# Kernel optimization log

Measured on AMD Instinct MI355X. Metric: run time of the kernel, lower is better.

The kernel has to match this reference:

```python
import jax, jax.numpy as jnp
import numpy as np

EPS = 1e-7
K_CURV = 1.0                       # init_curvature buffer
HOPFIELD_DIM = 128
BETA = 1.0 / HOPFIELD_DIM ** 0.5   # default beta = 1/sqrt(hopfield_dim)


def _to_tangent0(x):
    # prepend zero time coordinate, clip max norm to 3.5
    zeros = jnp.zeros(x.shape[:-1] + (1,), dtype=x.dtype)
    x = jnp.concatenate([zeros, x], axis=-1)
    n = jnp.linalg.norm(x, axis=-1, keepdims=True)
    factor = jnp.minimum(3.5 / (n + EPS), 1.0)
    return x * factor


def _linner(u, v):
    # Minkowski (Lorentz) inner product: -u0*v0 + sum_i ui*vi
    return -u[..., 0] * v[..., 0] + jnp.sum(u[..., 1:] * v[..., 1:], axis=-1)


def _expmap0(u, k):
    # exp map at hyperboloid origin; u has zero time component
    sk = jnp.sqrt(k)
    xs = u[..., 1:]
    n = jnp.maximum(jnp.linalg.norm(xs, axis=-1, keepdims=True), EPS)
    t = n / sk
    return jnp.concatenate([sk * jnp.cosh(t), sk * jnp.sinh(t) * xs / n], axis=-1)


def _logmap(x, y, k):
    # log map of y in tangent space at x
    xy = _linner(x, y)[..., None]
    dist = jnp.sqrt(k) * jnp.arccosh(jnp.maximum(-xy / k, 1.0 + EPS))
    nomin = y + (xy / k) * x
    denom = jnp.sqrt(jnp.maximum(_linner(nomin, nomin)[..., None], EPS))
    return dist * nomin / denom


def _expmap(x, u, k):
    # exp map of tangent vector u at base point x
    sk = jnp.sqrt(k)
    un = jnp.sqrt(jnp.maximum(_linner(u, u)[..., None], EPS))
    t = un / sk
    return jnp.cosh(t) * x + sk * jnp.sinh(t) * u / un


def _logmap0(x, k):
    # log map at origin; time component of the result is zero
    sk = jnp.sqrt(k)
    xs = x[..., 1:]
    n = jnp.maximum(jnp.linalg.norm(xs, axis=-1, keepdims=True), EPS)
    dist = sk * jnp.arccosh(jnp.maximum(x[..., :1] / sk, 1.0 + EPS))
    return jnp.concatenate([jnp.zeros_like(x[..., :1]), dist * xs / n], axis=-1)


def setup_inputs() -> dict:
    key = jax.random.key(0)
    k1, k2, k3, k4, k5 = jax.random.split(key, 5)
    N, M, D_MEM, D_H, D_OUT = 1024, 2048, 512, 128, 128
    return {
        "queries": jax.random.normal(k1, (N, D_H), dtype=jnp.float32),
        "keys": jax.random.normal(k2, (M, D_MEM), dtype=jnp.float32),
        "values": jax.random.normal(k3, (M, D_MEM), dtype=jnp.float32),
        "W_K": jax.random.normal(k4, (D_MEM, D_H), dtype=jnp.float32) * 0.05,
        "W_V": jax.random.normal(k5, (D_H, D_OUT), dtype=jnp.float32) * 0.05,
    }


def reference(queries, keys, values, W_K, W_V):
    k = K_CURV
    Q = _expmap0(_to_tangent0(queries), k)              # [N, D+1]
    K = _expmap0(_to_tangent0(keys @ W_K), k)           # [M, D+1]
    V = _expmap0(_to_tangent0((values @ W_K) @ W_V), k) # [M, D+1]
    sim = _linner(Q[:, None, :], K[None, :, :])         # [N, M]
    alpha = jax.nn.softmax(-BETA * sim, axis=-1)        # [N, M]
    log_values = _logmap(Q[:, None, :], V[None, :, :], k)  # [N, M, D+1]
    tangent_mean = jnp.sum(alpha[..., None] * log_values, axis=1)  # [N, D+1]
    z = _expmap(Q, tangent_mean, k)
    return _logmap0(z, k)[..., 1:]                      # [N, D]
```

## Files before the change

### kernel.cpp

```cpp
#include <hip/hip_runtime.h>
#include <math.h>

#define EPSF 1e-7f
#define BETA_F 0.08838834764831845f

typedef __attribute__((ext_vector_type(8))) short bf8_t;
typedef __attribute__((ext_vector_type(4))) float f32x4;

#define WS_QT    0
#define WS_LQ    1024
#define WS_KT    2048
#define WS_VTM   4096
#define WS_LV    6144
#define WS_QS    8192
#define WS_QHI   139264
#define WS_QLO   204800
#define WS_KHI   270336
#define WS_KLO   401408
#define WS_VHI   532480
#define WS_VLO   663552
#define WS_VTHI  794624
#define WS_VTLO  925696
#define WS_WKT0  1056768
#define WS_WKT1  1089536
#define WS_WKT2  1122304
#define WS_WVT0  1155072
#define WS_WVT1  1163264
#define WS_WVT2  1171456
#define WS_PART  1179648

__device__ __forceinline__ float wave_sum(float v) {
#pragma unroll
  for (int off = 32; off > 0; off >>= 1) v += __shfl_xor(v, off);
  return v;
}
__device__ __forceinline__ unsigned short f2bf(float x) {
  unsigned int u = __float_as_uint(x);
  u += 0x7FFFu + ((u >> 16) & 1u);
  return (unsigned short)(u >> 16);
}
__device__ __forceinline__ float bf2f(unsigned short h) {
  return __uint_as_float(((unsigned int)h) << 16);
}
__device__ __forceinline__ void split3(float x, unsigned short& s0, unsigned short& s1,
                                       unsigned short& s2) {
  s0 = f2bf(x);
  float r1 = x - bf2f(s0);
  s1 = f2bf(r1);
  s2 = f2bf(r1 - bf2f(s1));
}
__device__ __forceinline__ bf8_t ld8(const unsigned short* p) {
  return __builtin_bit_cast(bf8_t, *(const uint4*)p);
}
__device__ __forceinline__ f32x4 mfma16(bf8_t a, bf8_t b, f32x4 c) {
  return __builtin_amdgcn_mfma_f32_16x16x32_bf16(a, b, c, 0, 0, 0);
}

__global__ void prep_q(const float* __restrict__ queries, float* __restrict__ Qs,
                       float* __restrict__ qt, float* __restrict__ lqv,
                       unsigned int* __restrict__ Qhi, unsigned int* __restrict__ Qlo) {
  int i = blockIdx.x;
  int lane = threadIdx.x;
  float2 r = ((const float2*)(queries + (size_t)i * 128))[lane];
  float s2 = wave_sum(r.x * r.x + r.y * r.y);
  float n = sqrtf(s2);
  float f = fminf(3.5f / (n + EPSF), 1.0f);
  float t = fmaxf(n * f, EPSF);
  float coef = sinhf(t) / t * f;
  float ch = coshf(t);
  float x0 = coef * r.x, x1 = coef * r.y;
  ((float2*)(Qs + (size_t)i * 128))[lane] = make_float2(x0, x1);
  unsigned short h0 = f2bf(x0), h1 = f2bf(x1);
  Qhi[i * 64 + lane] = (unsigned)h0 | ((unsigned)h1 << 16);
  unsigned short g0 = f2bf(x0 - bf2f(h0)), g1 = f2bf(x1 - bf2f(h1));
  Qlo[i * 64 + lane] = (unsigned)g0 | ((unsigned)g1 << 16);
  if (lane == 0) {
    qt[i] = ch;
    lqv[i] = coef * coef * s2 - ch * ch;
  }
}

__global__ void convert_w(const float* __restrict__ WK, const float* __restrict__ WV,
                          unsigned short* __restrict__ WKT0, unsigned short* __restrict__ WKT1,
                          unsigned short* __restrict__ WKT2,
                          unsigned short* __restrict__ WVT0, unsigned short* __restrict__ WVT1,
                          unsigned short* __restrict__ WVT2) {
  int t = blockIdx.x * 256 + threadIdx.x;
  if (t < 65536) {
    int n = t >> 9, k = t & 511;
    unsigned short a, b, c;
    split3(WK[k * 128 + n], a, b, c);
    WKT0[t] = a; WKT1[t] = b; WKT2[t] = c;
  } else {
    int t2 = t - 65536;
    int n = t2 >> 7, k = t2 & 127;
    unsigned short a, b, c;
    split3(WV[k * 128 + n], a, b, c);
    WVT0[t2] = a; WVT1[t2] = b; WVT2[t2] = c;
  }
}

__launch_bounds__(512)
__global__ void prep_kv(const float* __restrict__ keys, const float* __restrict__ values,
                        const unsigned short* __restrict__ WKT0,
                        const unsigned short* __restrict__ WKT1,
                        const unsigned short* __restrict__ WKT2,
                        const unsigned short* __restrict__ WVT0,
                        const unsigned short* __restrict__ WVT1,
                        const unsigned short* __restrict__ WVT2,
                        unsigned short* __restrict__ Khi, unsigned short* __restrict__ Klo,
                        float* __restrict__ kt,
                        unsigned short* __restrict__ Vhi, unsigned short* __restrict__ Vlo,
                        unsigned short* __restrict__ VThi, unsigned short* __restrict__ VTlo,
                        float* __restrict__ vt, float* __restrict__ lv) {
  int tid = threadIdx.x, wv = tid >> 6, lane = tid & 63;
  int l15 = lane & 15, lh = lane >> 4;
  int b = blockIdx.x;
  bool isK = b < 128;
  int r0 = (b & 127) * 16;
  const float* src = isK ? keys : values;

  __shared__ __align__(16) float ldsD[16][132];
  __shared__ __align__(16) unsigned short v1p[3][16][128];
  __shared__ __align__(16) float ldsD2[16][132];
  __shared__ __align__(16) float ldsT[128][17];

  f32x4 acc = f32x4{0, 0, 0, 0};
  const float* arow = src + (size_t)(r0 + l15) * 512 + lh * 8;
#pragma unroll 2
  for (int ks = 0; ks < 16; ++ks) {
    float4 a0 = *(const float4*)(arow + ks * 32);
    float4 a1 = *(const float4*)(arow + ks * 32 + 4);
    float av[8] = {a0.x, a0.y, a0.z, a0.w, a1.x, a1.y, a1.z, a1.w};
    bf8_t aa0, aa1, aa2;
#pragma unroll
    for (int i = 0; i < 8; ++i) {
      unsigned short p0, p1, p2;
      split3(av[i], p0, p1, p2);
      aa0[i] = (short)p0; aa1[i] = (short)p1; aa2[i] = (short)p2;
    }
    size_t boff = (size_t)(wv * 16 + l15) * 512 + ks * 32 + lh * 8;
    bf8_t b0 = ld8(WKT0 + boff);
    bf8_t b1 = ld8(WKT1 + boff);
    bf8_t b2 = ld8(WKT2 + boff);
    acc = mfma16(aa0, b0, acc);
    acc = mfma16(aa0, b1, acc);
    acc = mfma16(aa1, b0, acc);
    acc = mfma16(aa0, b2, acc);
    acc = mfma16(aa1, b1, acc);
    acc = mfma16(aa2, b0, acc);
  }
#pragma unroll
  for (int r = 0; r < 4; ++r) ldsD[lh * 4 + r][wv * 16 + l15] = acc[r];
  __syncthreads();

  if (isK) {
    if (tid < 256) {
      int row = tid >> 4, l = tid & 15;
      float a[8];
#pragma unroll
      for (int n = 0; n < 8; ++n) a[n] = ldsD[row][n * 16 + l];
      float s2 = 0.f;
#pragma unroll
      for (int n = 0; n < 8; ++n) s2 += a[n] * a[n];
#pragma unroll
      for (int off = 1; off < 16; off <<= 1) s2 += __shfl_xor(s2, off);
      float nn = sqrtf(s2);
      float f = fminf(3.5f / (nn + EPSF), 1.0f);
      float t = fmaxf(nn * f, EPSF);
      float coef = sinhf(t) / t * f;
      if (l == 0) kt[r0 + row] = coshf(t);
#pragma unroll
      for (int n = 0; n < 8; ++n) {
        float sv = coef * a[n];
        unsigned short h = f2bf(sv);
        Khi[(size_t)(r0 + row) * 128 + n * 16 + l] = h;
        Klo[(size_t)(r0 + row) * 128 + n * 16 + l] = f2bf(sv - bf2f(h));
      }
    }
    return;
  }

  if (tid < 256) {
    int row = tid >> 4, l = tid & 15;
#pragma unroll
    for (int n = 0; n < 8; ++n) {
      unsigned short p0, p1, p2;
      split3(ldsD[row][n * 16 + l], p0, p1, p2);
      v1p[0][row][n * 16 + l] = p0;
      v1p[1][row][n * 16 + l] = p1;
      v1p[2][row][n * 16 + l] = p2;
    }
  }
  __syncthreads();

  f32x4 a2 = f32x4{0, 0, 0, 0};
#pragma unroll
  for (int ks = 0; ks < 4; ++ks) {
    bf8_t x0 = ld8(&v1p[0][l15][ks * 32 + lh * 8]);
    bf8_t x1 = ld8(&v1p[1][l15][ks * 32 + lh * 8]);
    bf8_t x2 = ld8(&v1p[2][l15][ks * 32 + lh * 8]);
    size_t boff = (size_t)(wv * 16 + l15) * 128 + ks * 32 + lh * 8;
    bf8_t b0 = ld8(WVT0 + boff);
    bf8_t b1 = ld8(WVT1 + boff);
    bf8_t b2 = ld8(WVT2 + boff);
    a2 = mfma16(x0, b0, a2);
    a2 = mfma16(x0, b1, a2);
    a2 = mfma16(x1, b0, a2);
    a2 = mfma16(x0, b2, a2);
    a2 = mfma16(x1, b1, a2);
    a2 = mfma16(x2, b0, a2);
  }
#pragma unroll
  for (int r = 0; r < 4; ++r) ldsD2[lh * 4 + r][wv * 16 + l15] = a2[r];
  __syncthreads();

  if (tid < 256) {
    int row = tid >> 4, l = tid & 15;
    float a[8];
#pragma unroll
    for (int n = 0; n < 8; ++n) a[n] = ldsD2[row][n * 16 + l];
    float s2 = 0.f;
#pragma unroll
    for (int n = 0; n < 8; ++n) s2 += a[n] * a[n];
#pragma unroll
    for (int off = 1; off < 16; off <<= 1) s2 += __shfl_xor(s2, off);
    float nn = sqrtf(s2);
    float f = fminf(3.5f / (nn + EPSF), 1.0f);
    float t = fmaxf(nn * f, EPSF);
    float coef = sinhf(t) / t * f;
    float ch = coshf(t);
    if (l == 0) {
      vt[r0 + row] = ch;
      lv[r0 + row] = coef * coef * s2 - ch * ch;
    }
#pragma unroll
    for (int n = 0; n < 8; ++n) {
      float sv = coef * a[n];
      unsigned short h = f2bf(sv);
      Vhi[(size_t)(r0 + row) * 128 + n * 16 + l] = h;
      Vlo[(size_t)(r0 + row) * 128 + n * 16 + l] = f2bf(sv - bf2f(h));
      ldsT[n * 16 + l][row] = sv;
    }
  }
  __syncthreads();

  if (tid < 128) {
    int d = tid;
    unsigned int wh[8], wl[8];
#pragma unroll
    for (int i = 0; i < 8; ++i) {
      float s0 = ldsT[d][2 * i], s1 = ldsT[d][2 * i + 1];
      unsigned short h0 = f2bf(s0), h1 = f2bf(s1);
      unsigned short g0 = f2bf(s0 - bf2f(h0)), g1 = f2bf(s1 - bf2f(h1));
      wh[i] = (unsigned)h0 | ((unsigned)h1 << 16);
      wl[i] = (unsigned)g0 | ((unsigned)g1 << 16);
    }
    size_t o = (size_t)d * 2048 + r0;
    *(uint4*)(VThi + o) = make_uint4(wh[0], wh[1], wh[2], wh[3]);
    *(uint4*)(VThi + o + 8) = make_uint4(wh[4], wh[5], wh[6], wh[7]);
    *(uint4*)(VTlo + o) = make_uint4(wl[0], wl[1], wl[2], wl[3]);
    *(uint4*)(VTlo + o + 8) = make_uint4(wl[4], wl[5], wl[6], wl[7]);
  }
}

__launch_bounds__(256, 2)
__global__ void attn_mfma(const unsigned short* __restrict__ Qhi, const unsigned short* __restrict__ Qlo,
                          const unsigned short* __restrict__ Khi, const unsigned short* __restrict__ Klo,
                          const unsigned short* __restrict__ Vhi, const unsigned short* __restrict__ Vlo,
                          const unsigned short* __restrict__ VThi, const unsigned short* __restrict__ VTlo,
                          const float* __restrict__ qt, const float* __restrict__ lqv,
                          const float* __restrict__ kt, const float* __restrict__ vt,
                          const float* __restrict__ lv, float* __restrict__ part) {
  int tid = threadIdx.x, wv = tid >> 6, lane = tid & 63;
  int l15 = lane & 15, lh = lane >> 4;
  int qg = blockIdx.x >> 3, sp = blockIdx.x & 7;
  int q0 = qg * 16;
  int j0 = sp * 256 + wv * 64;

  __shared__ __align__(16) unsigned short ghA[4][1024];
  __shared__ __align__(16) unsigned short glA[4][1024];
  __shared__ __align__(16) float mergeO[4][16][132];
  __shared__ float mergeS[4][3][16];

  bf8_t qfh[4], qfl[4];
  {
    const unsigned short* qp = Qhi + (size_t)(q0 + l15) * 128 + lh * 8;
    const unsigned short* ql = Qlo + (size_t)(q0 + l15) * 128 + lh * 8;
#pragma unroll
    for (int ks = 0; ks < 4; ++ks) { qfh[ks] = ld8(qp + ks * 32); qfl[ks] = ld8(ql + ks * 32); }
  }
  float qtr[4], lq2[4];
#pragma unroll
  for (int r = 0; r < 4; ++r) {
    int q = q0 + lh * 4 + r;
    qtr[r] = qt[q];
    lq2[r] = 2.0f + lqv[q];
  }
  float ktj[4], vtj[4], lvj[4];
#pragma unroll
  for (int n = 0; n < 4; ++n) {
    int j = j0 + n * 16 + l15;
    ktj[n] = kt[j]; vtj[n] = vt[j]; lvj[n] = lv[j];
  }

  auto loadT = [&](bf8_t* st, int nn) {
    size_t jrow = (size_t)(j0 + nn * 16 + l15) * 128 + lh * 8;
#pragma unroll
    for (int ks = 0; ks < 4; ++ks) {
      st[ks * 4 + 0] = ld8(Khi + jrow + ks * 32);
      st[ks * 4 + 1] = ld8(Klo + jrow + ks * 32);
      st[ks * 4 + 2] = ld8(Vhi + jrow + ks * 32);
      st[ks * 4 + 3] = ld8(Vlo + jrow + ks * 32);
    }
  };
  auto mfmaT = [&](const bf8_t* st, f32x4& s, f32x4& c) {
#pragma unroll
    for (int ks = 0; ks < 4; ++ks) {
      s = mfma16(qfh[ks], st[ks * 4 + 0], s);
      s = mfma16(qfh[ks], st[ks * 4 + 1], s);
      s = mfma16(qfl[ks], st[ks * 4 + 0], s);
      c = mfma16(qfh[ks], st[ks * 4 + 2], c);
      c = mfma16(qfh[ks], st[ks * 4 + 3], c);
      c = mfma16(qfl[ks], st[ks * 4 + 2], c);
    }
  };
  f32x4 sf[4], cf[4];
#pragma unroll
  for (int n = 0; n < 4; ++n) { sf[n] = f32x4{0, 0, 0, 0}; cf[n] = f32x4{0, 0, 0, 0}; }
  bf8_t stA[16], stB[16];
  loadT(stA, 0);
  loadT(stB, 1);
  mfmaT(stA, sf[0], cf[0]);
  loadT(stA, 2);
  mfmaT(stB, sf[1], cf[1]);
  loadT(stB, 3);
  mfmaT(stA, sf[2], cf[2]);
  mfmaT(stB, sf[3], cf[3]);

  bf8_t vA[16], vB[16];
  auto loadV = [&](bf8_t* st, int jk) {
#pragma unroll
    for (int dn = 0; dn < 8; ++dn) {
      size_t vrow = (size_t)(dn * 16 + l15) * 2048 + j0 + jk * 32 + lh * 8;
      st[dn * 2 + 0] = ld8(VThi + vrow);
      st[dn * 2 + 1] = ld8(VTlo + vrow);
    }
  };
  loadV(vA, 0);

  float lsum[4] = {0, 0, 0, 0}, tcs[4] = {0, 0, 0, 0}, tts[4] = {0, 0, 0, 0};
#pragma unroll
  for (int n = 0; n < 4; ++n) {
#pragma unroll
    for (int r = 0; r < 4; ++r) {
      float sim = sf[n][r] - qtr[r] * ktj[n];
      float c = cf[n][r] - qtr[r] * vtj[n];
      float e = expf(-BETA_F * sim);
      float z = fmaxf(-c, 1.0f + EPSF);
      float dist = acoshf(z);
      float den2 = fmaxf(lvj[n] + lq2[r] * c * c, EPSF);
      float g = e * dist * rsqrtf(den2);
      lsum[r] += e;
      tcs[r] += g * c;
      tts[r] += g * vtj[n];
      unsigned short gh = f2bf(g);
      unsigned short gl = f2bf(g - bf2f(gh));
      int q_ = lh * 4 + r;
      int idx = (q_ * 64 + n * 16 + l15) ^ ((q_ & 7) << 3);
      ghA[wv][idx] = gh;
      glA[wv][idx] = gl;
    }
  }
  loadV(vB, 1);
  asm volatile("s_waitcnt lgkmcnt(0)" ::: "memory");
  __builtin_amdgcn_sched_barrier(0);

  f32x4 accO[8];
#pragma unroll
  for (int dn = 0; dn < 8; ++dn) accO[dn] = f32x4{0, 0, 0, 0};
  {
    int base0 = (l15 * 64 + 0 * 32 + lh * 8) ^ ((l15 & 7) << 3);
    bf8_t ah = ld8(&ghA[wv][base0]);
    bf8_t al = ld8(&glA[wv][base0]);
#pragma unroll
    for (int dn = 0; dn < 8; ++dn) {
      accO[dn] = mfma16(ah, vA[dn * 2 + 0], accO[dn]);
      accO[dn] = mfma16(ah, vA[dn * 2 + 1], accO[dn]);
      accO[dn] = mfma16(al, vA[dn * 2 + 0], accO[dn]);
    }
  }
  {
    int base1 = (l15 * 64 + 1 * 32 + lh * 8) ^ ((l15 & 7) << 3);
    bf8_t ah = ld8(&ghA[wv][base1]);
    bf8_t al = ld8(&glA[wv][base1]);
#pragma unroll
    for (int dn = 0; dn < 8; ++dn) {
      accO[dn] = mfma16(ah, vB[dn * 2 + 0], accO[dn]);
      accO[dn] = mfma16(ah, vB[dn * 2 + 1], accO[dn]);
      accO[dn] = mfma16(al, vB[dn * 2 + 0], accO[dn]);
    }
  }

#pragma unroll
  for (int r = 0; r < 4; ++r) {
#pragma unroll
    for (int off = 1; off < 16; off <<= 1) {
      lsum[r] += __shfl_xor(lsum[r], off);
      tcs[r] += __shfl_xor(tcs[r], off);
      tts[r] += __shfl_xor(tts[r], off);
    }
  }

#pragma unroll
  for (int r = 0; r < 4; ++r) {
    int q_ = lh * 4 + r;
#pragma unroll
    for (int dn = 0; dn < 8; ++dn) mergeO[wv][q_][dn * 16 + l15] = accO[dn][r];
    if (l15 == 0) {
      mergeS[wv][0][q_] = lsum[r];
      mergeS[wv][1][q_] = tcs[r];
      mergeS[wv][2][q_] = tts[r];
    }
  }
  __syncthreads();

#pragma unroll
  for (int e = 0; e < 2; ++e) {
    int t = tid + e * 256;
    int q_ = t >> 5, d0 = (t & 31) * 4;
    float4 s = make_float4(0.f, 0.f, 0.f, 0.f);
#pragma unroll
    for (int w = 0; w < 4; ++w) {
      float4 v = *(const float4*)&mergeO[w][q_][d0];
      s.x += v.x; s.y += v.y; s.z += v.z; s.w += v.w;
    }
    float* P = part + ((size_t)(q0 + q_) * 8 + sp) * 132;
    *(float4*)(P + d0) = s;
  }
  if (tid < 16) {
    int q_ = tid;
    float a = 0, b = 0, cc2 = 0;
#pragma unroll
    for (int w = 0; w < 4; ++w) {
      a += mergeS[w][0][q_];
      b += mergeS[w][1][q_];
      cc2 += mergeS[w][2][q_];
    }
    float* P = part + ((size_t)(q0 + q_) * 8 + sp) * 132;
    P[128] = a; P[129] = b; P[130] = cc2;
  }
}

__global__ void merge_fin(const float* __restrict__ part, const float* __restrict__ Qs,
                          const float* __restrict__ qt, float* __restrict__ out) {
  int qi = blockIdx.x;
  int lane = threadIdx.x;
  const float* P = part + (size_t)qi * 8 * 132;
  float ox = 0, oy = 0, l = 0, tc = 0, tt = 0;
#pragma unroll
  for (int s = 0; s < 8; ++s) {
    const float* p = P + s * 132;
    float2 o2 = *(const float2*)(p + 2 * lane);
    ox += o2.x; oy += o2.y;
    l += p[128]; tc += p[129]; tt += p[130];
  }
  float2 q2 = ((const float2*)(Qs + (size_t)qi * 128))[lane];
  float qtv = qt[qi];
  float invl = 1.0f / l;
  float Tmx = (ox + tc * q2.x) * invl;
  float Tmy = (oy + tc * q2.y) * invl;
  float Tmt = (tt + tc * qtv) * invl;
  float sp2 = wave_sum(Tmx * Tmx + Tmy * Tmy);
  float LT = sp2 - Tmt * Tmt;
  float un = sqrtf(fmaxf(LT, EPSF));
  float ch = coshf(un);
  float shv = sinhf(un) / un;
  float zx = ch * q2.x + shv * Tmx;
  float zy = ch * q2.y + shv * Tmy;
  float zt = ch * qtv + shv * Tmt;
  float zn2 = wave_sum(zx * zx + zy * zy);
  float nz = fmaxf(sqrtf(zn2), EPSF);
  float dist = acoshf(fmaxf(zt, 1.0f + EPSF));
  float sc = dist / nz;
  ((float2*)(out + (size_t)qi * 128))[lane] = make_float2(sc * zx, sc * zy);
}

extern "C" void kernel_launch(void* const* d_in, const int* in_sizes, int n_in,
                              void* d_out, int out_size, void* d_ws, size_t ws_size,
                              hipStream_t stream) {
  const float* queries = (const float*)d_in[0];
  const float* keys = (const float*)d_in[1];
  const float* values = (const float*)d_in[2];
  const float* WK = (const float*)d_in[3];
  const float* WV = (const float*)d_in[4];
  float* ws = (float*)d_ws;

  float* qt_ = ws + WS_QT;
  float* lq_ = ws + WS_LQ;
  float* kt_ = ws + WS_KT;
  float* vt_ = ws + WS_VTM;
  float* lv_ = ws + WS_LV;
  float* Qs = ws + WS_QS;
  unsigned short* Qhi = (unsigned short*)(ws + WS_QHI);
  unsigned short* Qlo = (unsigned short*)(ws + WS_QLO);
  unsigned short* Khi = (unsigned short*)(ws + WS_KHI);
  unsigned short* Klo = (unsigned short*)(ws + WS_KLO);
  unsigned short* Vhi = (unsigned short*)(ws + WS_VHI);
  unsigned short* Vlo = (unsigned short*)(ws + WS_VLO);
  unsigned short* VThi = (unsigned short*)(ws + WS_VTHI);
  unsigned short* VTlo = (unsigned short*)(ws + WS_VTLO);
  unsigned short* WKT0 = (unsigned short*)(ws + WS_WKT0);
  unsigned short* WKT1 = (unsigned short*)(ws + WS_WKT1);
  unsigned short* WKT2 = (unsigned short*)(ws + WS_WKT2);
  unsigned short* WVT0 = (unsigned short*)(ws + WS_WVT0);
  unsigned short* WVT1 = (unsigned short*)(ws + WS_WVT1);
  unsigned short* WVT2 = (unsigned short*)(ws + WS_WVT2);
  float* part = ws + WS_PART;
  float* out = (float*)d_out;

  prep_q<<<1024, 64, 0, stream>>>(queries, Qs, qt_, lq_, (unsigned int*)Qhi, (unsigned int*)Qlo);
  convert_w<<<320, 256, 0, stream>>>(WK, WV, WKT0, WKT1, WKT2, WVT0, WVT1, WVT2);
  prep_kv<<<256, 512, 0, stream>>>(keys, values, WKT0, WKT1, WKT2, WVT0, WVT1, WVT2,
                                   Khi, Klo, kt_, Vhi, Vlo, VThi, VTlo, vt_, lv_);
  attn_mfma<<<512, 256, 0, stream>>>(Qhi, Qlo, Khi, Klo, Vhi, Vlo, VThi, VTlo,
                                     qt_, lq_, kt_, vt_, lv_, part);
  merge_fin<<<1024, 64, 0, stream>>>(part, Qs, qt_, out);
}
```

Before: 70.49 us.

## Halve prep_kv rows per block, tile weight transpose through LDS, prefetch A loads

Result: slower. 88.72 us (+25.9%).

```diff
diff --git a/kernel.cpp b/kernel.cpp
--- a/kernel.cpp
+++ b/kernel.cpp
@@ -85,18 +85,43 @@
                           unsigned short* __restrict__ WKT2,
                           unsigned short* __restrict__ WVT0, unsigned short* __restrict__ WVT1,
                           unsigned short* __restrict__ WVT2) {
-  int t = blockIdx.x * 256 + threadIdx.x;
-  if (t < 65536) {
-    int n = t >> 9, k = t & 511;
-    unsigned short a, b, c;
-    split3(WK[k * 128 + n], a, b, c);
-    WKT0[t] = a; WKT1[t] = b; WKT2[t] = c;
+  __shared__ float tile[64][65];
+  int b = blockIdx.x, tid = threadIdx.x;
+  if (b < 16) {
+    int kt = b >> 1, nt = b & 1;
+    int c0 = tid & 63, r0 = tid >> 6;
+#pragma unroll
+    for (int i = 0; i < 16; ++i) {
+      int kr = r0 + i * 4;
+      tile[kr][c0] = WK[(size_t)(kt * 64 + kr) * 128 + nt * 64 + c0];
+    }
+    __syncthreads();
+#pragma unroll
+    for (int i = 0; i < 16; ++i) {
+      int nr = r0 + i * 4;
+      unsigned short a, bb, c;
+      split3(tile[c0][nr], a, bb, c);
+      size_t o = (size_t)(nt * 64 + nr) * 512 + kt * 64 + c0;
+      WKT0[o] = a; WKT1[o] = bb; WKT2[o] = c;
+    }
   } else {
-    int t2 = t - 65536;
-    int n = t2 >> 7, k = t2 & 127;
-    unsigned short a, b, c;
-    split3(WV[k * 128 + n], a, b, c);
-    WVT0[t2] = a; WVT1[t2] = b; WVT2[t2] = c;
+    int b2 = b - 16;
+    int kt = b2 >> 1, nt = b2 & 1;
+    int c0 = tid & 63, r0 = tid >> 6;
+#pragma unroll
+    for (int i = 0; i < 16; ++i) {
+      int kr = r0 + i * 4;
+      tile[kr][c0] = WV[(size_t)(kt * 64 + kr) * 128 + nt * 64 + c0];
+    }
+    __syncthreads();
+#pragma unroll
+    for (int i = 0; i < 16; ++i) {
+      int nr = r0 + i * 4;
+      unsigned short a, bb, c;
+      split3(tile[c0][nr], a, bb, c);
+      size_t o = (size_t)(nt * 64 + nr) * 128 + kt * 64 + c0;
+      WVT0[o] = a; WVT1[o] = bb; WVT2[o] = c;
+    }
   }
 }
 
@@ -116,8 +141,8 @@
   int tid = threadIdx.x, wv = tid >> 6, lane = tid & 63;
   int l15 = lane & 15, lh = lane >> 4;
   int b = blockIdx.x;
-  bool isK = b < 128;
-  int r0 = (b & 127) * 16;
+  bool isK = b < 256;
+  int r0 = (b & 255) * 8;
   const float* src = isK ? keys : values;
 
   __shared__ __align__(16) float ldsD[16][132];
@@ -126,11 +151,16 @@
   __shared__ __align__(16) float ldsT[128][17];
 
   f32x4 acc = f32x4{0, 0, 0, 0};
-  const float* arow = src + (size_t)(r0 + l15) * 512 + lh * 8;
-#pragma unroll 2
+  const float* arow = src + (size_t)(r0 + (l15 & 7)) * 512 + lh * 8;
+  float4 pa0 = *(const float4*)(arow);
+  float4 pa1 = *(const float4*)(arow + 4);
+#pragma unroll
   for (int ks = 0; ks < 16; ++ks) {
-    float4 a0 = *(const float4*)(arow + ks * 32);
-    float4 a1 = *(const float4*)(arow + ks * 32 + 4);
+    float4 a0 = pa0, a1 = pa1;
+    if (ks < 15) {
+      pa0 = *(const float4*)(arow + (ks + 1) * 32);
+      pa1 = *(const float4*)(arow + (ks + 1) * 32 + 4);
+    }
     float av[8] = {a0.x, a0.y, a0.z, a0.w, a1.x, a1.y, a1.z, a1.w};
     bf8_t aa0, aa1, aa2;
 #pragma unroll
@@ -155,7 +185,7 @@
   __syncthreads();
 
   if (isK) {
-    if (tid < 256) {
+    if (tid < 128) {
       int row = tid >> 4, l = tid & 15;
       float a[8];
 #pragma unroll
@@ -181,7 +211,7 @@
     return;
   }
 
-  if (tid < 256) {
+  if (tid < 128) {
     int row = tid >> 4, l = tid & 15;
 #pragma unroll
     for (int n = 0; n < 8; ++n) {
@@ -190,6 +220,9 @@
       v1p[0][row][n * 16 + l] = p0;
       v1p[1][row][n * 16 + l] = p1;
       v1p[2][row][n * 16 + l] = p2;
+      v1p[0][row + 8][n * 16 + l] = p0;
+      v1p[1][row + 8][n * 16 + l] = p1;
+      v1p[2][row + 8][n * 16 + l] = p2;
     }
   }
   __syncthreads();
@@ -215,7 +248,7 @@
   for (int r = 0; r < 4; ++r) ldsD2[lh * 4 + r][wv * 16 + l15] = a2[r];
   __syncthreads();
 
-  if (tid < 256) {
+  if (tid < 128) {
     int row = tid >> 4, l = tid & 15;
     float a[8];
 #pragma unroll
@@ -247,9 +280,9 @@
 
   if (tid < 128) {
     int d = tid;
-    unsigned int wh[8], wl[8];
-#pragma unroll
-    for (int i = 0; i < 8; ++i) {
+    unsigned int wh[4], wl[4];
+#pragma unroll
+    for (int i = 0; i < 4; ++i) {
       float s0 = ldsT[d][2 * i], s1 = ldsT[d][2 * i + 1];
       unsigned short h0 = f2bf(s0), h1 = f2bf(s1);
       unsigned short g0 = f2bf(s0 - bf2f(h0)), g1 = f2bf(s1 - bf2f(h1));
@@ -258,9 +291,7 @@
     }
     size_t o = (size_t)d * 2048 + r0;
     *(uint4*)(VThi + o) = make_uint4(wh[0], wh[1], wh[2], wh[3]);
-    *(uint4*)(VThi + o + 8) = make_uint4(wh[4], wh[5], wh[6], wh[7]);
     *(uint4*)(VTlo + o) = make_uint4(wl[0], wl[1], wl[2], wl[3]);
-    *(uint4*)(VTlo + o + 8) = make_uint4(wl[4], wl[5], wl[6], wl[7]);
   }
 }
 
@@ -520,8 +551,8 @@
   float* out = (float*)d_out;
 
   prep_q<<<1024, 64, 0, stream>>>(queries, Qs, qt_, lq_, (unsigned int*)Qhi, (unsigned int*)Qlo);
-  convert_w<<<320, 256, 0, stream>>>(WK, WV, WKT0, WKT1, WKT2, WVT0, WVT1, WVT2);
-  prep_kv<<<256, 512, 0, stream>>>(keys, values, WKT0, WKT1, WKT2, WVT0, WVT1, WVT2,
+  convert_w<<<20, 256, 0, stream>>>(WK, WV, WKT0, WKT1, WKT2, WVT0, WVT1, WVT2);
+  prep_kv<<<512, 512, 0, stream>>>(keys, values, WKT0, WKT1, WKT2, WVT0, WVT1, WVT2,
                                    Khi, Klo, kt_, Vhi, Vlo, VThi, VTlo, vt_, lv_);
   attn_mfma<<<512, 256, 0, stream>>>(Qhi, Qlo, Khi, Klo, Vhi, Vlo, VThi, VTlo,
                                      qt_, lq_, kt_, vt_, lv_, part);
```
